# Performance work log

Hardware: AMD Instinct MI355X
Metric: run time of the kernel (lower is better)

The kernel has to match this reference:

```python
import jax, jax.numpy as jnp
import numpy as np

EEG_CH = 64      # eeg_channel_new
WIN = 128        # window_length
KEN = 10         # cnn_ken_num
CONV_H = 64      # cnn_conv_hight (stride/kernel height)


def setup_inputs() -> dict:
    key = jax.random.key(0)
    ks = jax.random.split(key, 11)
    n = jax.random.normal
    return {
        "x": n(ks[0], (1, 1, 66, 128), dtype=jnp.float32),
        # SE fcn: Linear(64,64) -> Tanh -> Linear(64,64) -> Sigmoid -> Softmax
        "se_w1": n(ks[1], (64, 64), dtype=jnp.float32) * 0.1,
        "se_b1": n(ks[2], (64,), dtype=jnp.float32) * 0.1,
        "se_w2": n(ks[3], (64, 64), dtype=jnp.float32) * 0.1,
        "se_b2": n(ks[4], (64,), dtype=jnp.float32) * 0.1,
        # Conv2d(1, 10, (64, 9), stride=(64, 1))
        "conv_w": n(ks[5], (10, 1, 64, 9), dtype=jnp.float32) * 0.05,
        "conv_b": n(ks[6], (10,), dtype=jnp.float32) * 0.05,
        # fcn: Linear(20,10) -> Sigmoid -> Linear(10,2) -> Softmax
        "fcn_w1": n(ks[7], (10, 20), dtype=jnp.float32) * 0.1,
        "fcn_b1": n(ks[8], (10,), dtype=jnp.float32) * 0.1,
        "fcn_w2": n(ks[9], (2, 10), dtype=jnp.float32) * 0.1,
        "fcn_b2": n(ks[10], (2,), dtype=jnp.float32) * 0.1,
    }


def _dot(a, b):
    # Faithful to torch: tensordot over dim 0 -> [64,1]; diag of non-square -> [1];
    # then broadcast-divide by per-column norms -> [64].
    temp = jnp.diagonal(jnp.tensordot(a, b, axes=[[0], [0]]))  # [1]
    norm_a = jnp.linalg.norm(a, axis=0)                        # [64]
    norm_b = jnp.linalg.norm(b, axis=0)                        # [1]
    return temp / (norm_a * norm_b)                            # [64]


def reference(x, se_w1, se_b1, se_w2, se_b2, conv_w, conv_b,
              fcn_w1, fcn_b1, fcn_w2, fcn_b2):
    eeg = x[:, :, 1:1 + EEG_CH, :]      # [1,1,64,128]
    wav_a = x[:, :, 0:1, :]             # [1,1,1,128]
    wav_b = x[:, :, -1:, :]             # [1,1,1,128]

    e2 = eeg.reshape(EEG_CH, WIN)       # [64,128]
    r_a = _dot(e2.T, wav_a.reshape(1, WIN).T)   # [64]
    r_b = _dot(e2.T, wav_b.reshape(1, WIN).T)   # [64]
    eeg_r = jnp.concatenate([r_a, r_b]).reshape(2, -1)  # [2,64]

    # SE channel attention
    h = jnp.tanh(eeg_r @ se_w1.T + se_b1)
    se_w = jax.nn.softmax(jax.nn.sigmoid(h @ se_w2.T + se_b2), axis=1)  # [2,64]
    sd = eeg.reshape(1, EEG_CH, WIN).transpose(1, 0, 2)  # [64,1,128]
    sd = jnp.concatenate([sd, sd], axis=0)               # [128,1,128]
    # (transpose(0,2) * w.view(1,-1)).transpose(0,2) == scale along doubled-channel dim
    eeg_se = (sd * se_w.reshape(-1)[:, None, None]).transpose(1, 0, 2)  # [1,128,128]

    y = eeg_se.reshape(1, 1, 2 * EEG_CH, WIN)            # [1,1,128,128]
    y = jax.lax.conv_general_dilated(
        y, conv_w, window_strides=(CONV_H, 1), padding='VALID',
        dimension_numbers=('NCHW', 'OIHW', 'NCHW'))       # [1,10,2,120]
    y = jax.nn.relu(y + conv_b[None, :, None, None])
    # AdaptiveAvgPool2d((2,1)): H already 2, mean over W
    y = jnp.mean(y, axis=3, keepdims=True)                # [1,10,2,1]
    y = y.reshape(1, -1)                                  # [1,20]

    h2 = jax.nn.sigmoid(y @ fcn_w1.T + fcn_b1)
    return jax.nn.softmax(h2 @ fcn_w2.T + fcn_b2, axis=1)  # [1,2]
```

## Files before the change

kernel.cpp:

```cpp
#include <hip/hip_runtime.h>
#include <math.h>

#define EEG_CH 64
#define WIN    128
#define ROWP   132
#define NROWS  66
#define KW     9
#define OUTW   120
#define NOUT   10
#define NH     2

__device__ __forceinline__ float readlane_f(float v, int l) {
    return __int_as_float(__builtin_amdgcn_readlane(__float_as_int(v), l));
}

__launch_bounds__(1024)
__global__ void cnn_fused(const float* __restrict__ xg,
                          const float* __restrict__ w1g, const float* __restrict__ b1g,
                          const float* __restrict__ w2g, const float* __restrict__ b2g,
                          const float* __restrict__ cwg, const float* __restrict__ cbg,
                          const float* __restrict__ f1w, const float* __restrict__ f1b,
                          const float* __restrict__ f2w, const float* __restrict__ f2b,
                          float* __restrict__ out)
{
    __shared__ float xl[NROWS * ROWP];
    __shared__ float rnorm[NROWS];
    __shared__ float nums[2];
    __shared__ float eeg_r_l[128];
    __shared__ float hl[128];
    __shared__ float se_flat[128];
    __shared__ float msum[NOUT * NH];

    const int tid  = threadIdx.x;
    const int ws   = tid >> 6;
    const int lane = tid & 63;

    for (int t = tid; t < NROWS * (WIN / 4); t += 1024) {
        const int row = t >> 5, c4 = t & 31;
        const float4 v = *(const float4*)(xg + row * WIN + c4 * 4);
        *(float4*)(xl + row * ROWP + c4 * 4) = v;
    }

    const int wu = __builtin_amdgcn_readfirstlane(ws);
    float wl[KW];
    if (wu < NOUT) {
        const float* __restrict__ cwo = cwg + wu * EEG_CH * KW + lane * KW;
        #pragma unroll
        for (int k = 0; k < KW; ++k) wl[k] = cwo[k];
    }
    __syncthreads();

    for (int row = ws; row < NROWS; row += 16) {
        float v0 = xl[row * ROWP + lane];
        float v1 = xl[row * ROWP + 64 + lane];
        float s  = v0 * v0 + v1 * v1;
        for (int off = 32; off > 0; off >>= 1) s += __shfl_xor(s, off, 64);
        if (lane == 0) rnorm[row] = sqrtf(s);
    }
    if (ws < 2) {
        const int wrow = (ws == 0) ? 0 : 65;
        float p = xl[ROWP + lane]      * xl[wrow * ROWP + lane]
                + xl[ROWP + 64 + lane] * xl[wrow * ROWP + 64 + lane];
        for (int off = 32; off > 0; off >>= 1) p += __shfl_xor(p, off, 64);
        if (lane == 0) nums[ws] = p;
    }
    __syncthreads();

    if (ws < 2) {
        const int r = ws, j = lane;
        {
            const float denom = rnorm[j + 1] * (r == 0 ? rnorm[0] : rnorm[65]);
            eeg_r_l[r * 64 + j] = nums[r] / denom;
        }
        {
            float acc = b1g[j];
            const float4* wr = (const float4*)(w1g + j * 64);
            const float4* er = (const float4*)(eeg_r_l + r * 64);
            #pragma unroll
            for (int i = 0; i < 16; ++i) {
                const float4 a = er[i], b = wr[i];
                acc += a.x * b.x + a.y * b.y + a.z * b.z + a.w * b.w;
            }
            hl[r * 64 + j] = tanhf(acc);
        }
        {
            float acc = b2g[j];
            const float4* wr = (const float4*)(w2g + j * 64);
            const float4* hr = (const float4*)(hl + r * 64);
            #pragma unroll
            for (int i = 0; i < 16; ++i) {
                const float4 a = hr[i], b = wr[i];
                acc += a.x * b.x + a.y * b.y + a.z * b.z + a.w * b.w;
            }
            float sg = 1.0f / (1.0f + expf(-acc));
            float mx = sg;
            for (int off = 32; off > 0; off >>= 1) mx = fmaxf(mx, __shfl_xor(mx, off, 64));
            float e = expf(sg - mx);
            float ss = e;
            for (int off = 32; off > 0; off >>= 1) ss += __shfl_xor(ss, off, 64);
            se_flat[r * 64 + j] = e / ss;
        }
    }
    __syncthreads();

    if (wu < NOUT) {
        const int o = wu;
        const float s0l = se_flat[lane];
        const float s1l = se_flat[64 + lane];
        const int wbase = (lane < 60) ? 2 * lane : 116;
        float a00 = 0.f, a01 = 0.f, a10 = 0.f, a11 = 0.f;

        #pragma unroll 4
        for (int i = 0; i < EEG_CH; ++i) {
            const float2* xp = (const float2*)(xl + (i + 1) * ROWP + wbase);
            const float2 x0 = xp[0], x1 = xp[1], x2 = xp[2], x3 = xp[3], x4 = xp[4];
            const float xw[10] = { x0.x, x0.y, x1.x, x1.y, x2.x, x2.y,
                                   x3.x, x3.y, x4.x, x4.y };
            float wk[KW];
            #pragma unroll
            for (int k = 0; k < KW; ++k) wk[k] = readlane_f(wl[k], i);
            const float s0 = readlane_f(s0l, i);
            const float s1 = readlane_f(s1l, i);

            float p0 = 0.f, p1 = 0.f;
            #pragma unroll
            for (int k = 0; k < KW; ++k) {
                p0 += xw[k]     * wk[k];
                p1 += xw[k + 1] * wk[k];
            }
            a00 += s0 * p0;  a01 += s0 * p1;
            a10 += s1 * p0;  a11 += s1 * p1;
        }

        const float bo = cbg[o];
        float r0 = fmaxf(a00 + bo, 0.f) + fmaxf(a01 + bo, 0.f);
        float r1 = fmaxf(a10 + bo, 0.f) + fmaxf(a11 + bo, 0.f);
        if (lane >= 60) { r0 = 0.f; r1 = 0.f; }
        for (int off = 32; off > 0; off >>= 1) {
            r0 += __shfl_xor(r0, off, 64);
            r1 += __shfl_xor(r1, off, 64);
        }
        if (lane == 0) {
            msum[o * NH + 0] = r0 * (1.0f / OUTW);
            msum[o * NH + 1] = r1 * (1.0f / OUTW);
        }
    }
    __syncthreads();

    if (ws == 0) {
        float h2v = 0.f;
        if (lane < 10) {
            float a = f1b[lane];
            #pragma unroll
            for (int p = 0; p < 20; ++p) a += msum[p] * f1w[lane * 20 + p];
            h2v = 1.0f / (1.0f + expf(-a));
        }
        float t0 = (lane < 10) ? h2v * f2w[lane]      : 0.f;
        float t1 = (lane < 10) ? h2v * f2w[10 + lane] : 0.f;
        for (int off = 32; off > 0; off >>= 1) {
            t0 += __shfl_xor(t0, off, 64);
            t1 += __shfl_xor(t1, off, 64);
        }
        if (lane == 0) {
            const float l0 = f2b[0] + t0, l1 = f2b[1] + t1;
            const float m  = fmaxf(l0, l1);
            const float e0 = expf(l0 - m), e1 = expf(l1 - m);
            out[0] = e0 / (e0 + e1);
            out[1] = e1 / (e0 + e1);
        }
    }
}

extern "C" void kernel_launch(void* const* d_in, const int* in_sizes, int n_in,
                              void* d_out, int out_size, void* d_ws, size_t ws_size,
                              hipStream_t stream) {
    (void)in_sizes; (void)n_in; (void)d_ws; (void)ws_size; (void)out_size;
    const float* xg  = (const float*)d_in[0];
    const float* w1  = (const float*)d_in[1];
    const float* b1  = (const float*)d_in[2];
    const float* w2  = (const float*)d_in[3];
    const float* b2  = (const float*)d_in[4];
    const float* cw  = (const float*)d_in[5];
    const float* cb  = (const float*)d_in[6];
    const float* f1w = (const float*)d_in[7];
    const float* f1b = (const float*)d_in[8];
    const float* f2w = (const float*)d_in[9];
    const float* f2b = (const float*)d_in[10];
    float* out = (float*)d_out;
    cnn_fused<<<dim3(1), dim3(1024), 0, stream>>>(xg, w1, b1, w2, b2, cw, cb,
                                                  f1w, f1b, f2w, f2b, out);
}
```

Before: 94.95 us.

## Split fused kernel into three launches and spread conv across blocks

Replaces the single-block fused kernel with three kernels: an SE-attention kernel that stages transposed FC weights in shared memory and uses readlane broadcasts, a conv kernel launched with one block per output channel and the channel sum split across waves, and a tiny head kernel. Intermediate SE weights and pooled sums pass through the global workspace. This spreads the conv work over several compute units, at the cost of two extra kernel launches and global round-trips between stages.

```diff
diff --git a/kernel.cpp b/kernel.cpp
--- a/kernel.cpp
+++ b/kernel.cpp
@@ -3,178 +3,191 @@
 
 #define EEG_CH 64
 #define WIN    128
-#define ROWP   132
-#define NROWS  66
 #define KW     9
 #define OUTW   120
 #define NOUT   10
-#define NH     2
+#define ROWP   132
+
+#define WS_SE   0
+#define WS_MSUM 128
 
 __device__ __forceinline__ float readlane_f(float v, int l) {
     return __int_as_float(__builtin_amdgcn_readlane(__float_as_int(v), l));
 }
 
 __launch_bounds__(1024)
-__global__ void cnn_fused(const float* __restrict__ xg,
-                          const float* __restrict__ w1g, const float* __restrict__ b1g,
-                          const float* __restrict__ w2g, const float* __restrict__ b2g,
-                          const float* __restrict__ cwg, const float* __restrict__ cbg,
-                          const float* __restrict__ f1w, const float* __restrict__ f1b,
-                          const float* __restrict__ f2w, const float* __restrict__ f2b,
-                          float* __restrict__ out)
+__global__ void cnn_k1(const float* __restrict__ xg,
+                       const float* __restrict__ w1g, const float* __restrict__ b1g,
+                       const float* __restrict__ w2g, const float* __restrict__ b2g,
+                       float* __restrict__ wsout)
 {
-    __shared__ float xl[NROWS * ROWP];
-    __shared__ float rnorm[NROWS];
+    __shared__ float w1l[64 * 64];
+    __shared__ float w2l[64 * 64];
+    __shared__ float rnorm[66];
     __shared__ float nums[2];
-    __shared__ float eeg_r_l[128];
-    __shared__ float hl[128];
-    __shared__ float se_flat[128];
-    __shared__ float msum[NOUT * NH];
 
     const int tid  = threadIdx.x;
-    const int ws   = tid >> 6;
+    const int wv   = tid >> 6;
     const int lane = tid & 63;
 
-    for (int t = tid; t < NROWS * (WIN / 4); t += 1024) {
+    if (wv >= 8) {
+        const bool second = (wv >= 12);
+        const float* __restrict__ src = second ? w2g : w1g;
+        float* __restrict__ dst = second ? w2l : w1l;
+        const int t0 = (wv & 3) * 64 + lane;
+        for (int t = t0; t < 1024; t += 256) {
+            const int j  = t & 63;
+            const int i4 = t >> 6;
+            const float4 v = *(const float4*)(src + j * 64 + i4 * 4);
+            dst[(i4 * 4 + 0) * 64 + j] = v.x;
+            dst[(i4 * 4 + 1) * 64 + j] = v.y;
+            dst[(i4 * 4 + 2) * 64 + j] = v.z;
+            dst[(i4 * 4 + 3) * 64 + j] = v.w;
+        }
+    } else {
+        for (int row = wv; row < 66; row += 8) {
+            const float v0 = xg[row * WIN + lane];
+            const float v1 = xg[row * WIN + 64 + lane];
+            float s = v0 * v0 + v1 * v1;
+            for (int off = 32; off > 0; off >>= 1) s += __shfl_xor(s, off, 64);
+            if (lane == 0) rnorm[row] = sqrtf(s);
+        }
+        if (wv < 2) {
+            const int wrow = (wv == 0) ? 0 : 65;
+            float p = xg[WIN + lane]      * xg[wrow * WIN + lane]
+                    + xg[WIN + 64 + lane] * xg[wrow * WIN + 64 + lane];
+            for (int off = 32; off > 0; off >>= 1) p += __shfl_xor(p, off, 64);
+            if (lane == 0) nums[wv] = p;
+        }
+    }
+    __syncthreads();
+
+    if (wv < 2) {
+        const int r = wv, j = lane;
+        const float er = nums[r] / (rnorm[j + 1] * (r == 0 ? rnorm[0] : rnorm[65]));
+        float acc = b1g[j];
+        #pragma unroll
+        for (int i = 0; i < 64; ++i)
+            acc += readlane_f(er, i) * w1l[i * 64 + j];
+        const float hv = tanhf(acc);
+        float acc2 = b2g[j];
+        #pragma unroll
+        for (int i = 0; i < 64; ++i)
+            acc2 += readlane_f(hv, i) * w2l[i * 64 + j];
+        const float sg = 1.f / (1.f + expf(-acc2));
+        float mx = sg;
+        for (int off = 32; off > 0; off >>= 1) mx = fmaxf(mx, __shfl_xor(mx, off, 64));
+        const float e = expf(sg - mx);
+        float ss = e;
+        for (int off = 32; off > 0; off >>= 1) ss += __shfl_xor(ss, off, 64);
+        wsout[WS_SE + r * 64 + j] = e / ss;
+    }
+}
+
+__launch_bounds__(256)
+__global__ void cnn_k2(const float* __restrict__ xg,
+                       const float* __restrict__ cwg, const float* __restrict__ cbg,
+                       float* __restrict__ wsio)
+{
+    __shared__ float xl[64 * ROWP];
+    __shared__ float part[4][OUTW];
+
+    const int tid  = threadIdx.x;
+    const int wv   = tid >> 6;
+    const int lane = tid & 63;
+    const int o    = blockIdx.x;
+
+    for (int t = tid; t < 2048; t += 256) {
         const int row = t >> 5, c4 = t & 31;
-        const float4 v = *(const float4*)(xg + row * WIN + c4 * 4);
+        const float4 v = *(const float4*)(xg + (row + 1) * WIN + c4 * 4);
         *(float4*)(xl + row * ROWP + c4 * 4) = v;
     }
 
-    const int wu = __builtin_amdgcn_readfirstlane(ws);
+    const int h = wv >> 1, ihalf = wv & 1;
+    const int chbase = ihalf * 32;
     float wl[KW];
-    if (wu < NOUT) {
-        const float* __restrict__ cwo = cwg + wu * EEG_CH * KW + lane * KW;
+    float sl = 0.f;
+    if (lane < 32) {
+        const float* __restrict__ cwo = cwg + o * (EEG_CH * KW) + (chbase + lane) * KW;
         #pragma unroll
         for (int k = 0; k < KW; ++k) wl[k] = cwo[k];
+        sl = wsio[WS_SE + h * 64 + chbase + lane];
     }
     __syncthreads();
 
-    for (int row = ws; row < NROWS; row += 16) {
-        float v0 = xl[row * ROWP + lane];
-        float v1 = xl[row * ROWP + 64 + lane];
-        float s  = v0 * v0 + v1 * v1;
-        for (int off = 32; off > 0; off >>= 1) s += __shfl_xor(s, off, 64);
-        if (lane == 0) rnorm[row] = sqrtf(s);
-    }
-    if (ws < 2) {
-        const int wrow = (ws == 0) ? 0 : 65;
-        float p = xl[ROWP + lane]      * xl[wrow * ROWP + lane]
-                + xl[ROWP + 64 + lane] * xl[wrow * ROWP + 64 + lane];
-        for (int off = 32; off > 0; off >>= 1) p += __shfl_xor(p, off, 64);
-        if (lane == 0) nums[ws] = p;
+    const int wbase = (lane < 60) ? 2 * lane : 116;
+    float q0 = 0.f, q1 = 0.f;
+    #pragma unroll 4
+    for (int ii = 0; ii < 32; ++ii) {
+        const int i = chbase + ii;
+        const float2* xp = (const float2*)(xl + i * ROWP + wbase);
+        const float2 x0 = xp[0], x1 = xp[1], x2 = xp[2], x3 = xp[3], x4 = xp[4];
+        const float xw[10] = { x0.x, x0.y, x1.x, x1.y, x2.x, x2.y,
+                               x3.x, x3.y, x4.x, x4.y };
+        float wk[KW];
+        #pragma unroll
+        for (int k = 0; k < KW; ++k) wk[k] = readlane_f(wl[k], ii);
+        const float s = readlane_f(sl, ii);
+        float p0 = 0.f, p1 = 0.f;
+        #pragma unroll
+        for (int k = 0; k < KW; ++k) {
+            p0 += xw[k]     * wk[k];
+            p1 += xw[k + 1] * wk[k];
+        }
+        q0 += s * p0;
+        q1 += s * p1;
+    }
+    if (lane < 60) {
+        *(float2*)(&part[wv][wbase]) = make_float2(q0, q1);
     }
     __syncthreads();
 
-    if (ws < 2) {
-        const int r = ws, j = lane;
-        {
-            const float denom = rnorm[j + 1] * (r == 0 ? rnorm[0] : rnorm[65]);
-            eeg_r_l[r * 64 + j] = nums[r] / denom;
-        }
-        {
-            float acc = b1g[j];
-            const float4* wr = (const float4*)(w1g + j * 64);
-            const float4* er = (const float4*)(eeg_r_l + r * 64);
-            #pragma unroll
-            for (int i = 0; i < 16; ++i) {
-                const float4 a = er[i], b = wr[i];
-                acc += a.x * b.x + a.y * b.y + a.z * b.z + a.w * b.w;
-            }
-            hl[r * 64 + j] = tanhf(acc);
-        }
-        {
-            float acc = b2g[j];
-            const float4* wr = (const float4*)(w2g + j * 64);
-            const float4* hr = (const float4*)(hl + r * 64);
-            #pragma unroll
-            for (int i = 0; i < 16; ++i) {
-                const float4 a = hr[i], b = wr[i];
-                acc += a.x * b.x + a.y * b.y + a.z * b.z + a.w * b.w;
-            }
-            float sg = 1.0f / (1.0f + expf(-acc));
-            float mx = sg;
-            for (int off = 32; off > 0; off >>= 1) mx = fmaxf(mx, __shfl_xor(mx, off, 64));
-            float e = expf(sg - mx);
-            float ss = e;
-            for (int off = 32; off > 0; off >>= 1) ss += __shfl_xor(ss, off, 64);
-            se_flat[r * 64 + j] = e / ss;
-        }
-    }
-    __syncthreads();
-
-    if (wu < NOUT) {
-        const int o = wu;
-        const float s0l = se_flat[lane];
-        const float s1l = se_flat[64 + lane];
-        const int wbase = (lane < 60) ? 2 * lane : 116;
-        float a00 = 0.f, a01 = 0.f, a10 = 0.f, a11 = 0.f;
-
-        #pragma unroll 4
-        for (int i = 0; i < EEG_CH; ++i) {
-            const float2* xp = (const float2*)(xl + (i + 1) * ROWP + wbase);
-            const float2 x0 = xp[0], x1 = xp[1], x2 = xp[2], x3 = xp[3], x4 = xp[4];
-            const float xw[10] = { x0.x, x0.y, x1.x, x1.y, x2.x, x2.y,
-                                   x3.x, x3.y, x4.x, x4.y };
-            float wk[KW];
-            #pragma unroll
-            for (int k = 0; k < KW; ++k) wk[k] = readlane_f(wl[k], i);
-            const float s0 = readlane_f(s0l, i);
-            const float s1 = readlane_f(s1l, i);
-
-            float p0 = 0.f, p1 = 0.f;
-            #pragma unroll
-            for (int k = 0; k < KW; ++k) {
-                p0 += xw[k]     * wk[k];
-                p1 += xw[k + 1] * wk[k];
-            }
-            a00 += s0 * p0;  a01 += s0 * p1;
-            a10 += s1 * p0;  a11 += s1 * p1;
-        }
-
+    if (wv < 2) {
         const float bo = cbg[o];
-        float r0 = fmaxf(a00 + bo, 0.f) + fmaxf(a01 + bo, 0.f);
-        float r1 = fmaxf(a10 + bo, 0.f) + fmaxf(a11 + bo, 0.f);
-        if (lane >= 60) { r0 = 0.f; r1 = 0.f; }
-        for (int off = 32; off > 0; off >>= 1) {
-            r0 += __shfl_xor(r0, off, 64);
-            r1 += __shfl_xor(r1, off, 64);
-        }
-        if (lane == 0) {
-            msum[o * NH + 0] = r0 * (1.0f / OUTW);
-            msum[o * NH + 1] = r1 * (1.0f / OUTW);
-        }
-    }
-    __syncthreads();
-
-    if (ws == 0) {
-        float h2v = 0.f;
-        if (lane < 10) {
-            float a = f1b[lane];
-            #pragma unroll
-            for (int p = 0; p < 20; ++p) a += msum[p] * f1w[lane * 20 + p];
-            h2v = 1.0f / (1.0f + expf(-a));
-        }
-        float t0 = (lane < 10) ? h2v * f2w[lane]      : 0.f;
-        float t1 = (lane < 10) ? h2v * f2w[10 + lane] : 0.f;
-        for (int off = 32; off > 0; off >>= 1) {
-            t0 += __shfl_xor(t0, off, 64);
-            t1 += __shfl_xor(t1, off, 64);
-        }
-        if (lane == 0) {
-            const float l0 = f2b[0] + t0, l1 = f2b[1] + t1;
-            const float m  = fmaxf(l0, l1);
-            const float e0 = expf(l0 - m), e1 = expf(l1 - m);
-            out[0] = e0 / (e0 + e1);
-            out[1] = e1 / (e0 + e1);
-        }
+        float r = 0.f;
+        if (lane < 60) {
+            const float v0 = part[wv * 2][wbase]     + part[wv * 2 + 1][wbase]     + bo;
+            const float v1 = part[wv * 2][wbase + 1] + part[wv * 2 + 1][wbase + 1] + bo;
+            r = fmaxf(v0, 0.f) + fmaxf(v1, 0.f);
+        }
+        for (int off = 32; off > 0; off >>= 1) r += __shfl_xor(r, off, 64);
+        if (lane == 0) wsio[WS_MSUM + o * 2 + wv] = r * (1.0f / OUTW);
+    }
+}
+
+__launch_bounds__(64)
+__global__ void cnn_k3(const float* __restrict__ wsin,
+                       const float* __restrict__ f1w, const float* __restrict__ f1b,
+                       const float* __restrict__ f2w, const float* __restrict__ f2b,
+                       float* __restrict__ out)
+{
+    const int lane = threadIdx.x;
+    float h2v = 0.f;
+    if (lane < 10) {
+        float a = f1b[lane];
+        #pragma unroll
+        for (int p = 0; p < 20; ++p) a += wsin[WS_MSUM + p] * f1w[lane * 20 + p];
+        h2v = 1.f / (1.f + expf(-a));
+    }
+    float t0 = (lane < 10) ? h2v * f2w[lane]      : 0.f;
+    float t1 = (lane < 10) ? h2v * f2w[10 + lane] : 0.f;
+    for (int off = 32; off > 0; off >>= 1) {
+        t0 += __shfl_xor(t0, off, 64);
+        t1 += __shfl_xor(t1, off, 64);
+    }
+    if (lane == 0) {
+        const float l0 = f2b[0] + t0, l1 = f2b[1] + t1;
+        const float m  = fmaxf(l0, l1);
+        const float e0 = expf(l0 - m), e1 = expf(l1 - m);
+        out[0] = e0 / (e0 + e1);
+        out[1] = e1 / (e0 + e1);
     }
 }
 
 extern "C" void kernel_launch(void* const* d_in, const int* in_sizes, int n_in,
                               void* d_out, int out_size, void* d_ws, size_t ws_size,
                               hipStream_t stream) {
-    (void)in_sizes; (void)n_in; (void)d_ws; (void)ws_size; (void)out_size;
+    (void)in_sizes; (void)n_in; (void)ws_size; (void)out_size;
     const float* xg  = (const float*)d_in[0];
     const float* w1  = (const float*)d_in[1];
     const float* b1  = (const float*)d_in[2];
@@ -187,6 +200,9 @@
     const float* f2w = (const float*)d_in[9];
     const float* f2b = (const float*)d_in[10];
     float* out = (float*)d_out;
-    cnn_fused<<<dim3(1), dim3(1024), 0, stream>>>(xg, w1, b1, w2, b2, cw, cb,
-                                                  f1w, f1b, f2w, f2b, out);
-}
+    float* wsf = (float*)d_ws;
+
+    cnn_k1<<<dim3(1),    dim3(1024), 0, stream>>>(xg, w1, b1, w2, b2, wsf);
+    cnn_k2<<<dim3(NOUT), dim3(256),  0, stream>>>(xg, cw, cb, wsf);
+    cnn_k3<<<dim3(1),    dim3(64),   0, stream>>>(wsf, f1w, f1b, f2w, f2b, out);
+}
```

New measurement: 88.53 us. 6.8% less time.
